# Kernel tuning notes

Hardware: AMD Instinct MI355X
Metric: run time of the kernel (lower is better)

## Reference

```python
import jax, jax.numpy as jnp
import numpy as np

LN_EPS = 1e-6  # flax LayerNorm default


def setup_inputs() -> dict:
    B, S, D, H, HD = 4, 2048, 1024, 16, 64
    key = jax.random.key(0)
    ks = jax.random.split(key, 3)
    x = jax.random.normal(ks[0], (B, S, D), dtype=jnp.float32)
    mask = jnp.tril(jnp.ones((S, S), dtype=bool))[None, None]  # causal [1,1,S,S]
    ln_scale = jnp.ones((D,), jnp.float32)
    ln_bias = jnp.zeros((D,), jnp.float32)
    w_qkv = jax.random.normal(ks[1], (D, H, 3 * HD), jnp.float32) * (1.0 / np.sqrt(D))
    b_qkv = jnp.zeros((H, 3 * HD), jnp.float32)
    w_out = jax.random.normal(ks[2], (D, D), jnp.float32) * (1.0 / np.sqrt(D))
    b_out = jnp.zeros((D,), jnp.float32)
    return {"x": x, "mask": mask, "ln_scale": ln_scale, "ln_bias": ln_bias,
            "w_qkv": w_qkv, "b_qkv": b_qkv, "w_out": w_out, "b_out": b_out}


def _layernorm(x, scale, bias):
    mu = jnp.mean(x, axis=-1, keepdims=True)
    var = jnp.var(x, axis=-1, keepdims=True)
    return (x - mu) * jax.lax.rsqrt(var + LN_EPS) * scale + bias


def reference(x, mask, ln_scale, ln_bias, w_qkv, b_qkv, w_out, b_out):
    B, S, D = x.shape
    xn = _layernorm(x, ln_scale, ln_bias)                      # [B,S,D]
    qkv = jnp.einsum('bsd,dhf->bshf', xn, w_qkv) + b_qkv        # [B,S,H,3*hd]
    q, k, v = jnp.split(qkv, 3, axis=-1)                        # each [B,S,H,hd]
    scale = q.shape[-1] ** (-0.5)
    q = q * scale
    q = q.transpose(0, 2, 1, 3)                                 # [B,H,S,hd]
    k = k.transpose(0, 2, 1, 3)
    v = v.transpose(0, 2, 1, 3)
    attn = q @ k.swapaxes(-2, -1)                               # [B,H,S,S]
    attn = jnp.where(mask, attn, jnp.finfo(jnp.float32).min)
    attn = jax.nn.softmax(attn, axis=-1)
    y = attn @ v                                                # [B,H,S,hd]
    y = y.transpose(0, 2, 1, 3).reshape(B, S, D)
    y = y @ w_out + b_out                                       # [B,S,D]
    return y
```

## Files before the change

kernel.cpp:

```cpp
#include <hip/hip_runtime.h>

typedef unsigned short u16;
typedef unsigned int u32;
typedef __bf16 bf16x8 __attribute__((ext_vector_type(8)));
typedef float f32x4 __attribute__((ext_vector_type(4)));
typedef u16 u16x8 __attribute__((ext_vector_type(8)));
typedef u16 u16x4 __attribute__((ext_vector_type(4)));

#define GLOBAL_AS __attribute__((address_space(1)))
#define LDS_AS __attribute__((address_space(3)))

#define LOG2E 1.4426950408889634f
#define SMAX_C2 34.62468097703102f

__device__ __forceinline__ void async16(const u16* g, u16* l) {
  __builtin_amdgcn_global_load_lds((const GLOBAL_AS void*)g, (LDS_AS void*)l, 16, 0, 0);
}

__device__ __forceinline__ float bf2f(u16 u) {
  union { unsigned int i; float f; } v; v.i = ((unsigned int)u) << 16; return v.f;
}
__device__ __forceinline__ u16 f2bf(float f) {
  __bf16 h = (__bf16)f;
  return __builtin_bit_cast(u16, h);
}

__device__ __forceinline__ int swz(int r, int c) {
  return r * 64 + (c ^ ((r & 7) << 3));
}

__global__ __launch_bounds__(256) void prep_k(const float* __restrict__ x,
                                              const float* __restrict__ gamma,
                                              const float* __restrict__ beta,
                                              u16* __restrict__ xn,
                                              const float* __restrict__ wq,
                                              u16* __restrict__ wTq,
                                              const float* __restrict__ wo,
                                              u16* __restrict__ wTo) {
  __shared__ u16 tile[32][33];
  __shared__ float red[8];
  int id = blockIdx.x;
  if (id < 8192) {
    const int t = threadIdx.x, wid = t >> 6, lane = t & 63;
    const float* xr = x + (size_t)id * 1024;
    float4 v = *(const float4*)&xr[t * 4];
    float s = v.x + v.y + v.z + v.w;
    float ss = v.x * v.x + v.y * v.y + v.z * v.z + v.w * v.w;
    #pragma unroll
    for (int off = 32; off >= 1; off >>= 1) {
      s += __shfl_xor(s, off, 64);
      ss += __shfl_xor(ss, off, 64);
    }
    if (lane == 0) { red[wid] = s; red[4 + wid] = ss; }
    __syncthreads();
    s = red[0] + red[1] + red[2] + red[3];
    ss = red[4] + red[5] + red[6] + red[7];
    const float mu = s * (1.0f / 1024.0f);
    const float var = ss * (1.0f / 1024.0f) - mu * mu;
    const float rstd = rsqrtf(var + 1e-6f);
    float4 gv = *(const float4*)&gamma[t * 4];
    float4 bv = *(const float4*)&beta[t * 4];
    ushort4 o;
    o.x = f2bf((v.x - mu) * rstd * gv.x + bv.x);
    o.y = f2bf((v.y - mu) * rstd * gv.y + bv.y);
    o.z = f2bf((v.z - mu) * rstd * gv.z + bv.z);
    o.w = f2bf((v.w - mu) * rstd * gv.w + bv.w);
    *(ushort4*)&xn[(size_t)id * 1024 + t * 4] = o;
    return;
  }
  id -= 8192;
  const float* in; u16* out; int R, C, bx, by;
  if (id < 3072) { in = wq; out = wTq; R = 1024; C = 3072; bx = id % 96; by = id / 96; }
  else { id -= 3072; in = wo; out = wTo; R = 1024; C = 1024; bx = id & 31; by = id >> 5; }
  const int c0 = bx * 32, r0 = by * 32;
  const int tx = threadIdx.x & 31, ty = threadIdx.x >> 5;
  #pragma unroll
  for (int i = 0; i < 32; i += 8)
    tile[ty + i][tx] = f2bf(in[(size_t)(r0 + ty + i) * C + c0 + tx]);
  __syncthreads();
  #pragma unroll
  for (int i = 0; i < 32; i += 8)
    out[(size_t)(c0 + ty + i) * R + r0 + tx] = tile[tx][ty + i];
}

template <typename OutT>
__global__ __launch_bounds__(256) void gemm_bt(const u16* __restrict__ A,
                                               const u16* __restrict__ Bt,
                                               const float* __restrict__ bias,
                                               OutT* __restrict__ C,
                                               int M, int N, int K) {
  __shared__ __align__(16) u16 smem[24576];
  u16* As = smem;
  u16* Bs = smem + 12288;
  const int tid = threadIdx.x, wid = tid >> 6, lane = tid & 63;
  const int row = lane & 15, q4 = lane >> 4;
  const int m0 = blockIdx.y * 128, n0 = blockIdx.x * 128;
  const int wm = (wid >> 1) * 64, wn = (wid & 1) * 64;
  f32x4 acc[4][4] = {};
  const int sr = wid * 16 + (lane >> 2);
  const int sk = (((lane & 3) ^ ((lane >> 3) & 3))) * 8;
  const int xr = ((lane & 15) >> 1) & 3;
  const u16* gA0 = A + (size_t)(m0 + sr) * K + sk;
  const u16* gA1 = A + (size_t)(m0 + 64 + sr) * K + sk;
  const u16* gB0 = Bt + (size_t)(n0 + sr) * K + sk;
  const u16* gB1 = Bt + (size_t)(n0 + 64 + sr) * K + sk;
  const int lw = wid * 512;
  const int NT = K >> 5;

  async16(gA0, &As[lw]);
  async16(gA1, &As[2048 + lw]);
  async16(gB0, &Bs[lw]);
  async16(gB1, &Bs[2048 + lw]);
  async16(gA0 + 32, &As[4096 + lw]);
  async16(gA1 + 32, &As[4096 + 2048 + lw]);
  async16(gB0 + 32, &Bs[4096 + lw]);
  async16(gB1 + 32, &Bs[4096 + 2048 + lw]);

  int bc = 0, bs = 2;
  for (int kt = 0; kt < NT; ++kt) {
    if (kt + 1 < NT)
      asm volatile("s_waitcnt vmcnt(4)" ::: "memory");
    else
      asm volatile("s_waitcnt vmcnt(0)" ::: "memory");
    __builtin_amdgcn_s_barrier();
    __builtin_amdgcn_sched_barrier(0);
    if (kt + 2 < NT) {
      const int k0 = (kt + 2) << 5;
      async16(gA0 + k0, &As[bs * 4096 + lw]);
      async16(gA1 + k0, &As[bs * 4096 + 2048 + lw]);
      async16(gB0 + k0, &Bs[bs * 4096 + lw]);
      async16(gB1 + k0, &Bs[bs * 4096 + 2048 + lw]);
    }
    __builtin_amdgcn_sched_barrier(0);
    bf16x8 af[4], bfv[4];
    #pragma unroll
    for (int mt = 0; mt < 4; ++mt)
      af[mt] = *(const bf16x8*)
          &As[bc * 4096 + (wm + mt * 16 + row) * 32 + ((q4 ^ xr) * 8)];
    #pragma unroll
    for (int nt = 0; nt < 4; ++nt)
      bfv[nt] = *(const bf16x8*)
          &Bs[bc * 4096 + (wn + nt * 16 + row) * 32 + ((q4 ^ xr) * 8)];
    #pragma unroll
    for (int mt = 0; mt < 4; ++mt)
      #pragma unroll
      for (int nt = 0; nt < 4; ++nt)
        acc[mt][nt] = __builtin_amdgcn_mfma_f32_16x16x32_bf16(
            af[mt], bfv[nt], acc[mt][nt], 0, 0, 0);
    bs = bc;
    bc = (bc + 1 == 3) ? 0 : bc + 1;
  }

  if constexpr (sizeof(OutT) == 2) {
    __syncthreads();
    #pragma unroll
    for (int nt = 0; nt < 4; ++nt) {
      const float bv = bias[n0 + wn + nt * 16 + row];
      #pragma unroll
      for (int mt = 0; mt < 4; ++mt)
        #pragma unroll
        for (int r = 0; r < 4; ++r)
          smem[(wm + mt * 16 + q4 * 4 + r) * 136 + wn + nt * 16 + row] =
              f2bf(acc[mt][nt][r] + bv);
    }
    __syncthreads();
    const int rr = tid >> 1, cc = (tid & 1) * 64;
    const u16* src = &smem[rr * 136 + cc];
    u16* dst = (u16*)C + (size_t)(m0 + rr) * N + n0 + cc;
    #pragma unroll
    for (int j = 0; j < 8; ++j)
      *(u16x8*)&dst[j * 8] = *(const u16x8*)&src[j * 8];
  } else {
    #pragma unroll
    for (int nt = 0; nt < 4; ++nt) {
      const int gn = n0 + wn + nt * 16 + row;
      const float bv = bias[gn];
      #pragma unroll
      for (int mt = 0; mt < 4; ++mt) {
        const int gm = m0 + wm + mt * 16 + q4 * 4;
        #pragma unroll
        for (int r = 0; r < 4; ++r)
          C[(size_t)(gm + r) * N + gn] = (OutT)(acc[mt][nt][r] + bv);
      }
    }
  }
}

__global__ __launch_bounds__(256, 3) void attn_k(const u16* __restrict__ qkv,
                                                 u16* __restrict__ y) {
  __shared__ __align__(16) u16 Ks[2][64 * 64];
  __shared__ __align__(16) u16 Vs[2][64 * 64];
  __shared__ __align__(16) u16 Ps[4][2][16 * 64];
  const int tid = threadIdx.x, wid = tid >> 6, lane = tid & 63;
  const int row = lane & 15, q4 = lane >> 4;
  const int id = blockIdx.x;
  const int qb = 15 - (id >> 6);
  const int h = (id & 63) >> 2, b = id & 3;
  const size_t seq0 = (size_t)b * 2048;
  const u16* base = qkv + seq0 * 3072 + h * 192;
  const int kk = tid >> 2, ko = tid & 3;
  const int kp = tid & 31, dg = tid >> 5;

  bf16x8 ones;
  #pragma unroll
  for (int j = 0; j < 8; ++j) ones[j] = (__bf16)1.0f;

  const int rgmin = qb * 128 + wid * 32;
  const int rgmax = rgmin + 31;
  bf16x8 qf[2][2];
  #pragma unroll
  for (int g = 0; g < 2; ++g) {
    const u16* qp = base + (size_t)(rgmin + g * 16 + row) * 3072;
    qf[g][0] = *(const bf16x8*)(qp + q4 * 8);
    qf[g][1] = *(const bf16x8*)(qp + 32 + q4 * 8);
    #pragma unroll
    for (int j = 0; j < 8; ++j) {
      qf[g][0][j] = (__bf16)((float)qf[g][0][j] * 0.125f);
      qf[g][1][j] = (__bf16)((float)qf[g][1][j] * 0.125f);
    }
  }
  f32x4 l4[2] = {};
  f32x4 o[2][4] = {};
  const int ktiles = 2 * qb + 2;

  const u16* kg = base + (size_t)kk * 3072 + 64 + ko * 8;
  const u16* vg = base + (size_t)(2 * kp) * 3072 + 128 + dg * 8;
  u16x8 kr0 = *(const u16x8*)kg;
  u16x8 kr1 = *(const u16x8*)(kg + 32);
  u16x8 va = *(const u16x8*)vg;
  u16x8 vb = *(const u16x8*)(vg + 3072);
  *(u16x8*)&Ks[0][swz(kk, ko * 8)] = kr0;
  *(u16x8*)&Ks[0][swz(kk, ko * 8 + 32)] = kr1;
  #pragma unroll
  for (int j = 0; j < 8; ++j)
    *(u32*)&Vs[0][swz(dg * 8 + j, 2 * kp)] = (u32)va[j] | ((u32)vb[j] << 16);
  if (ktiles > 1) {
    kr0 = *(const u16x8*)(kg + (size_t)64 * 3072);
    kr1 = *(const u16x8*)(kg + (size_t)64 * 3072 + 32);
    va = *(const u16x8*)(vg + (size_t)64 * 3072);
    vb = *(const u16x8*)(vg + (size_t)65 * 3072);
  }
  __syncthreads();

  for (int kt = 0; kt < ktiles; ++kt) {
    const int kbase = kt * 64;
    const int cur = kt & 1;
    if (kt + 1 < ktiles) {
      *(u16x8*)&Ks[cur ^ 1][swz(kk, ko * 8)] = kr0;
      *(u16x8*)&Ks[cur ^ 1][swz(kk, ko * 8 + 32)] = kr1;
      #pragma unroll
      for (int j = 0; j < 8; ++j)
        *(u32*)&Vs[cur ^ 1][swz(dg * 8 + j, 2 * kp)] =
            (u32)va[j] | ((u32)vb[j] << 16);
      if (kt + 2 < ktiles) {
        const size_t nb = (size_t)(kbase + 128) * 3072;
        kr0 = *(const u16x8*)(kg + nb);
        kr1 = *(const u16x8*)(kg + nb + 32);
        va = *(const u16x8*)(vg + nb);
        vb = *(const u16x8*)(vg + nb + 3072);
      }
    }

    if (kbase <= rgmax) {
      #pragma unroll
      for (int nt = 0; nt < 4; ++nt) {
        bf16x8 kf0 = *(const bf16x8*)&Ks[cur][swz(nt * 16 + row, q4 * 8)];
        bf16x8 kf1 = *(const bf16x8*)&Ks[cur][swz(nt * 16 + row, 32 + q4 * 8)];
        #pragma unroll
        for (int g = 0; g < 2; ++g) {
          f32x4 z = {0.f, 0.f, 0.f, 0.f};
          z = __builtin_amdgcn_mfma_f32_16x16x32_bf16(qf[g][0], kf0, z, 0, 0, 0);
          z = __builtin_amdgcn_mfma_f32_16x16x32_bf16(qf[g][1], kf1, z, 0, 0, 0);
          const int rb = rgmin + g * 16;
          const bool mn = (kbase + 63 > rb);
          const int d = kbase + nt * 16 + row - rb - q4 * 4;
          u16* pw = Ps[wid][g];
          #pragma unroll
          for (int r = 0; r < 4; ++r) {
            const float bias = (mn && d > r) ? -1e30f : -SMAX_C2;
            const float p = __builtin_amdgcn_exp2f(fmaf(z[r], LOG2E, bias));
            pw[swz(q4 * 4 + r, nt * 16 + row)] = f2bf(p);
          }
        }
      }

      bf16x8 pf[2][2];
      #pragma unroll
      for (int g = 0; g < 2; ++g) {
        pf[g][0] = *(const bf16x8*)&Ps[wid][g][swz(row, q4 * 8)];
        pf[g][1] = *(const bf16x8*)&Ps[wid][g][swz(row, 32 + q4 * 8)];
        l4[g] = __builtin_amdgcn_mfma_f32_16x16x32_bf16(pf[g][0], ones, l4[g], 0, 0, 0);
        l4[g] = __builtin_amdgcn_mfma_f32_16x16x32_bf16(pf[g][1], ones, l4[g], 0, 0, 0);
      }

      #pragma unroll
      for (int t = 0; t < 4; ++t) {
        bf16x8 vf0 = *(const bf16x8*)&Vs[cur][swz(t * 16 + row, q4 * 8)];
        bf16x8 vf1 = *(const bf16x8*)&Vs[cur][swz(t * 16 + row, 32 + q4 * 8)];
        #pragma unroll
        for (int g = 0; g < 2; ++g) {
          o[g][t] = __builtin_amdgcn_mfma_f32_16x16x32_bf16(pf[g][0], vf0, o[g][t], 0, 0, 0);
          o[g][t] = __builtin_amdgcn_mfma_f32_16x16x32_bf16(pf[g][1], vf1, o[g][t], 0, 0, 0);
        }
      }
    }
    __syncthreads();
  }

  #pragma unroll
  for (int g = 0; g < 2; ++g) {
    const int srow = rgmin + g * 16 + q4 * 4;
    float inv[4];
    #pragma unroll
    for (int r = 0; r < 4; ++r) inv[r] = 1.0f / l4[g][r];
    #pragma unroll
    for (int t = 0; t < 4; ++t)
      #pragma unroll
      for (int r = 0; r < 4; ++r)
        y[(seq0 + srow + r) * 1024 + h * 64 + t * 16 + row] =
            f2bf(o[g][t][r] * inv[r]);
  }
}

extern "C" void kernel_launch(void* const* d_in, const int* in_sizes, int n_in,
                              void* d_out, int out_size, void* d_ws, size_t ws_size,
                              hipStream_t stream) {
  const float* x     = (const float*)d_in[0];
  const float* ln_s  = (const float*)d_in[2];
  const float* ln_b  = (const float*)d_in[3];
  const float* w_qkv = (const float*)d_in[4];
  const float* b_qkv = (const float*)d_in[5];
  const float* w_out = (const float*)d_in[6];
  const float* b_out = (const float*)d_in[7];
  float* out = (float*)d_out;

  u16* qkv   = (u16*)d_ws;
  u16* xn    = qkv + (size_t)8192 * 3072;
  u16* wTq   = xn + (size_t)8192 * 1024;
  u16* wTo   = wTq + (size_t)3072 * 1024;
  u16* yattn = xn;

  prep_k<<<12288, 256, 0, stream>>>(x, ln_s, ln_b, xn, w_qkv, wTq, w_out, wTo);
  gemm_bt<u16><<<dim3(24, 64), 256, 0, stream>>>(xn, wTq, b_qkv, qkv, 8192, 3072, 1024);
  attn_k<<<1024, 256, 0, stream>>>(qkv, yattn);
  gemm_bt<float><<<dim3(8, 64), 256, 0, stream>>>(yattn, wTo, b_out, out, 8192, 1024, 1024);
}
```

Measured before the change: 265.0 us.

## Use 256x256-tile triple-buffered GEMM kernel for QKV projection

Adds a new bf16 MFMA GEMM kernel with 256x256 block tiles, 512 threads (8 waves each computing 128x64), and a three-stage async global-to-LDS pipeline. It replaces the 128x128 kernel for the QKV projection. The larger tile raises arithmetic intensity and cuts global/L2 traffic per FLOP. In exchange it uses 96KB of LDS and 128 accumulator registers per lane, which may limit occupancy. The grid shrinks to 384 blocks on a 256-CU device, which can leave a partial second wave.

```diff
diff --git a/kernel.cpp b/kernel.cpp
--- a/kernel.cpp
+++ b/kernel.cpp
@@ -81,6 +81,87 @@
   #pragma unroll
   for (int i = 0; i < 32; i += 8)
     out[(size_t)(c0 + ty + i) * R + r0 + tx] = tile[tx][ty + i];
+}
+
+__global__ __launch_bounds__(512, 2) void gemm256_bt(const u16* __restrict__ A,
+                                                     const u16* __restrict__ Bt,
+                                                     const float* __restrict__ bias,
+                                                     u16* __restrict__ C,
+                                                     int M, int N, int K) {
+  __shared__ __align__(16) u16 smem[49152];
+  u16* As = smem;
+  u16* Bs = smem + 24576;
+  const int tid = threadIdx.x, wid = tid >> 6, lane = tid & 63;
+  const int row = lane & 15, q4 = lane >> 4;
+  const int m0 = blockIdx.y * 256, n0 = blockIdx.x * 256;
+  const int wm = (wid >> 2) * 128, wn = (wid & 3) * 64;
+  f32x4 acc[8][4] = {};
+  const int sr = tid >> 2;
+  const int sk = (((tid & 3) ^ ((tid >> 3) & 3))) * 8;
+  const int xr = ((lane & 15) >> 1) & 3;
+  const u16* gA0 = A + (size_t)(m0 + sr) * K + sk;
+  const u16* gA1 = gA0 + (size_t)128 * K;
+  const u16* gB0 = Bt + (size_t)(n0 + sr) * K + sk;
+  const u16* gB1 = gB0 + (size_t)128 * K;
+  const int ld = tid * 8;
+  const int NT = K >> 5;
+
+  async16(gA0, &As[ld]);
+  async16(gA1, &As[4096 + ld]);
+  async16(gB0, &Bs[ld]);
+  async16(gB1, &Bs[4096 + ld]);
+  async16(gA0 + 32, &As[8192 + ld]);
+  async16(gA1 + 32, &As[8192 + 4096 + ld]);
+  async16(gB0 + 32, &Bs[8192 + ld]);
+  async16(gB1 + 32, &Bs[8192 + 4096 + ld]);
+
+  int bc = 0, bs = 2;
+  for (int kt = 0; kt < NT; ++kt) {
+    if (kt + 1 < NT)
+      asm volatile("s_waitcnt vmcnt(4)" ::: "memory");
+    else
+      asm volatile("s_waitcnt vmcnt(0)" ::: "memory");
+    __builtin_amdgcn_s_barrier();
+    __builtin_amdgcn_sched_barrier(0);
+    if (kt + 2 < NT) {
+      const int k0 = (kt + 2) << 5;
+      async16(gA0 + k0, &As[bs * 8192 + ld]);
+      async16(gA1 + k0, &As[bs * 8192 + 4096 + ld]);
+      async16(gB0 + k0, &Bs[bs * 8192 + ld]);
+      async16(gB1 + k0, &Bs[bs * 8192 + 4096 + ld]);
+    }
+    __builtin_amdgcn_sched_barrier(0);
+    bf16x8 af[8], bfv[4];
+    #pragma unroll
+    for (int mt = 0; mt < 8; ++mt)
+      af[mt] = *(const bf16x8*)
+          &As[bc * 8192 + (wm + mt * 16 + row) * 32 + ((q4 ^ xr) * 8)];
+    #pragma unroll
+    for (int nt = 0; nt < 4; ++nt)
+      bfv[nt] = *(const bf16x8*)
+          &Bs[bc * 8192 + (wn + nt * 16 + row) * 32 + ((q4 ^ xr) * 8)];
+    #pragma unroll
+    for (int mt = 0; mt < 8; ++mt)
+      #pragma unroll
+      for (int nt = 0; nt < 4; ++nt)
+        acc[mt][nt] = __builtin_amdgcn_mfma_f32_16x16x32_bf16(
+            af[mt], bfv[nt], acc[mt][nt], 0, 0, 0);
+    bs = bc;
+    bc = (bc + 1 == 3) ? 0 : bc + 1;
+  }
+
+  #pragma unroll
+  for (int nt = 0; nt < 4; ++nt) {
+    const int gn = n0 + wn + nt * 16 + row;
+    const float bv = bias[gn];
+    #pragma unroll
+    for (int mt = 0; mt < 8; ++mt) {
+      const int gm = m0 + wm + mt * 16 + q4 * 4;
+      #pragma unroll
+      for (int r = 0; r < 4; ++r)
+        C[(size_t)(gm + r) * N + gn] = f2bf(acc[mt][nt][r] + bv);
+    }
+  }
 }
 
 template <typename OutT>
@@ -341,7 +422,7 @@
   u16* yattn = xn;
 
   prep_k<<<12288, 256, 0, stream>>>(x, ln_s, ln_b, xn, w_qkv, wTq, w_out, wTo);
-  gemm_bt<u16><<<dim3(24, 64), 256, 0, stream>>>(xn, wTq, b_qkv, qkv, 8192, 3072, 1024);
+  gemm256_bt<<<dim3(12, 32), 512, 0, stream>>>(xn, wTq, b_qkv, qkv, 8192, 3072, 1024);
   attn_k<<<1024, 256, 0, stream>>>(qkv, yattn);
   gemm_bt<float><<<dim3(8, 64), 256, 0, stream>>>(yattn, wTo, b_out, out, 8192, 1024, 1024);
 }
```

New measurement: 267.3 us. About the same (+0.9%).

## Use 256x256-tile phased MFMA GEMM with interleaved async prefetch for QKV projection

Applied to the files above, without the earlier changes.

Replaces the 128x128 QKV projection GEMM with a 256x256 tile kernel using 512 threads, 128 KB of LDS double-buffered via global_load_lds, and four phases per K step. Each phase interleaves issuing next-tile loads with MFMA work, using explicit waitcnt, barriers and setprio. The aim is more data reuse per loaded byte and better overlap of memory with compute. The cost is fewer blocks (384) on the GPU, heavy LDS use that limits occupancy, and a strided per-element bf16 store epilogue.

```diff
diff --git a/kernel.cpp b/kernel.cpp
--- a/kernel.cpp
+++ b/kernel.cpp
@@ -81,6 +81,118 @@
   #pragma unroll
   for (int i = 0; i < 32; i += 8)
     out[(size_t)(c0 + ty + i) * R + r0 + tx] = tile[tx][ty + i];
+}
+
+__global__ __launch_bounds__(512, 2) void gemm256_ph(const u16* __restrict__ A,
+                                                     const u16* __restrict__ Bt,
+                                                     const float* __restrict__ bias,
+                                                     u16* __restrict__ C,
+                                                     int M, int N, int K) {
+  __shared__ __align__(16) u16 smem[65536];
+  const int tid = threadIdx.x, wid = tid >> 6, lane = tid & 63;
+  const int row = lane & 15, q4 = lane >> 4;
+  const int m0 = blockIdx.y * 256, n0 = blockIdx.x * 256;
+  const int arow = (wid >> 2) * 128;
+  const int brow = (wid & 3) * 64;
+  const int xq = (q4 ^ ((row >> 1) & 3)) * 8;
+  f32x4 acc[8][4] = {};
+
+  const int r1g = (wid & 3) + ((wid >> 2) << 3);
+  const int r2g = r1g + 4;
+  const int bg0 = 2 * wid, bg1 = 2 * wid + 1;
+  const int lrow = lane >> 2;
+  const int lc = ((lane & 3) ^ ((lane >> 3) & 3)) * 8;
+  const int l8 = lane * 8;
+  const u16* pa1 = A + (size_t)(m0 + r1g * 16 + lrow) * K + lc;
+  const u16* pa2 = A + (size_t)(m0 + r2g * 16 + lrow) * K + lc;
+  const u16* pb0 = Bt + (size_t)(n0 + bg0 * 16 + lrow) * K + lc;
+  const u16* pb1 = Bt + (size_t)(n0 + bg1 * 16 + lrow) * K + lc;
+  const int NT = K >> 6;
+
+  {
+    u16* aL = &smem[0];
+    u16* bL = &smem[32768];
+    async16(pa1, aL + r1g * 512 + l8);
+    async16(pb0, bL + bg0 * 512 + l8);
+    async16(pb1, bL + bg1 * 512 + l8);
+    async16(pa2, aL + r2g * 512 + l8);
+    async16(pa1 + 32, aL + 8192 + r1g * 512 + l8);
+    async16(pb0 + 32, bL + 8192 + bg0 * 512 + l8);
+    async16(pb1 + 32, bL + 8192 + bg1 * 512 + l8);
+    async16(pa2 + 32, aL + 8192 + r2g * 512 + l8);
+  }
+  asm volatile("s_waitcnt vmcnt(5)" ::: "memory");
+  __builtin_amdgcn_s_barrier();
+
+  int buf = 0;
+  for (int kk = 0; kk < NT; ++kk) {
+    const int nbuf = buf ^ 1;
+    u16* aLn = &smem[nbuf * 16384];
+    u16* bLn = &smem[32768 + nbuf * 16384];
+    const int koff = (kk + 1) << 6;
+    bf16x8 bfv[4];
+    #pragma unroll
+    for (int ph = 0; ph < 4; ++ph) {
+      const int mhl = ph & 1, ks = ph >> 1;
+      bf16x8 af[4];
+      const u16* Ab = &smem[buf * 16384 + ks * 8192];
+      #pragma unroll
+      for (int i = 0; i < 4; ++i)
+        af[i] = *(const bf16x8*)&Ab[(arow + mhl * 64 + i * 16 + row) * 32 + xq];
+      if (mhl == 0) {
+        const u16* Bb = &smem[32768 + buf * 16384 + ks * 8192];
+        #pragma unroll
+        for (int j = 0; j < 4; ++j)
+          bfv[j] = *(const bf16x8*)&Bb[(brow + j * 16 + row) * 32 + xq];
+      }
+      __builtin_amdgcn_sched_barrier(0);
+      if (kk + 1 < NT) {
+        if (ph == 0) {
+          async16(pa1 + koff, aLn + r1g * 512 + l8);
+          async16(pb0 + koff, bLn + bg0 * 512 + l8);
+        } else if (ph == 1) {
+          async16(pb1 + koff, bLn + bg1 * 512 + l8);
+          async16(pa2 + koff, aLn + r2g * 512 + l8);
+        } else if (ph == 2) {
+          async16(pa1 + koff + 32, aLn + 8192 + r1g * 512 + l8);
+          async16(pb0 + koff + 32, bLn + 8192 + bg0 * 512 + l8);
+        } else {
+          async16(pb1 + koff + 32, bLn + 8192 + bg1 * 512 + l8);
+          async16(pa2 + koff + 32, aLn + 8192 + r2g * 512 + l8);
+        }
+        asm volatile("s_waitcnt vmcnt(5)" ::: "memory");
+      } else {
+        if (ph == 0) asm volatile("s_waitcnt vmcnt(4)" ::: "memory");
+        else if (ph == 1) asm volatile("s_waitcnt vmcnt(1)" ::: "memory");
+        else if (ph == 2) asm volatile("s_waitcnt vmcnt(0)" ::: "memory");
+      }
+      __builtin_amdgcn_s_barrier();
+      __builtin_amdgcn_sched_barrier(0);
+      __builtin_amdgcn_s_setprio(1);
+      #pragma unroll
+      for (int i = 0; i < 4; ++i)
+        #pragma unroll
+        for (int j = 0; j < 4; ++j)
+          acc[mhl * 4 + i][j] = __builtin_amdgcn_mfma_f32_16x16x32_bf16(
+              af[i], bfv[j], acc[mhl * 4 + i][j], 0, 0, 0);
+      __builtin_amdgcn_s_setprio(0);
+      __builtin_amdgcn_s_barrier();
+    }
+    buf = nbuf;
+  }
+
+  #pragma unroll
+  for (int nt = 0; nt < 4; ++nt) {
+    const int gn = n0 + brow + nt * 16 + row;
+    const float bv = bias[gn];
+    #pragma unroll
+    for (int mt = 0; mt < 8; ++mt) {
+      const int gm = m0 + arow + mt * 16 + q4 * 4;
+      #pragma unroll
+      for (int r = 0; r < 4; ++r)
+        C[(size_t)(gm + r) * N + gn] = f2bf(acc[mt][nt][r] + bv);
+    }
+  }
 }
 
 template <typename OutT>
@@ -341,7 +453,7 @@
   u16* yattn = xn;
 
   prep_k<<<12288, 256, 0, stream>>>(x, ln_s, ln_b, xn, w_qkv, wTq, w_out, wTo);
-  gemm_bt<u16><<<dim3(24, 64), 256, 0, stream>>>(xn, wTq, b_qkv, qkv, 8192, 3072, 1024);
+  gemm256_ph<<<dim3(12, 32), 512, 0, stream>>>(xn, wTq, b_qkv, qkv, 8192, 3072, 1024);
   attn_k<<<1024, 256, 0, stream>>>(qkv, yattn);
   gemm_bt<float><<<dim3(8, 64), 256, 0, stream>>>(yattn, wTo, b_out, out, 8192, 1024, 1024);
 }
```

After: 265.7 us. No clear change (+0.3%).
